# Performance work log

Measured on AMD Instinct MI355X. Metric: run time of the kernel, lower is better.

Reference implementation:

```python
import jax, jax.numpy as jnp
import numpy as np

N = 8192
IN_F = 512
OUT_F = 64
ALPHA = 0.2  # LeakyReLU negative slope
NEG_INF = -9e15


def setup_inputs() -> dict:
    key = jax.random.key(0)
    k1, k2, k3, k4 = jax.random.split(key, 4)
    # xavier_uniform-style scale (gain=1.414)
    w_bound = 1.414 * np.sqrt(6.0 / (IN_F + OUT_F))
    a_bound = 1.414 * np.sqrt(6.0 / (2 * OUT_F + 1))
    return {
        "input": jax.random.normal(k1, (N, IN_F), dtype=jnp.float32),
        "adj": jax.random.randint(k2, (N, N), 0, 2, dtype=jnp.int32),
        "W": jax.random.uniform(k3, (IN_F, OUT_F), jnp.float32, -w_bound, w_bound),
        "a": jax.random.uniform(k4, (2 * OUT_F, 1), jnp.float32, -a_bound, a_bound),
        "sig_sample_size": 512,
    }


def reference(input, adj, W, a, sig_sample_size):
    h = input @ W  # [N, F]
    # Split 'a' so e_ij = leakyrelu(a1.h_i + a2.h_j) without the N*N*2F repeat/cat
    a1, a2 = a[:OUT_F, 0], a[OUT_F:, 0]  # [F], [F]
    e = jax.nn.leaky_relu((h @ a1)[:, None] + (h @ a2)[None, :], negative_slope=ALPHA)  # [N, N]
    attention = jnp.where(adj > 0, e, NEG_INF)
    attention = jax.nn.softmax(attention, axis=1)
    sig_scores = jnp.sum(attention, axis=0)  # [N]
    _, indices = jax.lax.top_k(sig_scores, sig_sample_size)
    return indices
```

## Files before the change

### kernel.cpp

```cpp
#include <hip/hip_runtime.h>
#include <stdint.h>

#define NROW 8192
#define IN_F 512
#define OUT_F 64
#define ALPHA 0.2f

__device__ float  g_wa1[IN_F];
__device__ float  g_wa2[IN_F];
__device__ float  g_f1[NROW];
__device__ float  g_f2[NROW];
__device__ float  g_E2f[NROW];
__device__ float  g_F2f[NROW];
__device__ double g_E2d[NROW];
__device__ double g_F2d[NROW];
__device__ double g_accp[NROW];
__device__ double g_accn[NROW];
__device__ double g_G1[NROW];
__device__ double g_H1[NROW];
__device__ double g_colsum[NROW];
__device__ unsigned long long g_mask[(size_t)NROW * 128];

__global__ void prep_wa(const float* __restrict__ W, const float* __restrict__ a) {
    int k = threadIdx.x;
    if (k < IN_F) {
        double s1 = 0.0, s2 = 0.0;
        for (int t = 0; t < OUT_F; ++t) {
            double w = (double)W[k * OUT_F + t];
            s1 += w * (double)a[t];
            s2 += w * (double)a[OUT_F + t];
        }
        g_wa1[k] = (float)s1;
        g_wa2[k] = (float)s2;
        #pragma unroll
        for (int i = 0; i < 16; ++i) g_colsum[k * 16 + i] = 0.0;
    }
}

__global__ void __launch_bounds__(256) compute_f(const float* __restrict__ in) {
    int wave = threadIdx.x >> 6, lane = threadIdx.x & 63;
    int row = blockIdx.x * 4 + wave;
    const float4* in4  = (const float4*)(in + (size_t)row * IN_F);
    const float4* wa14 = (const float4*)g_wa1;
    const float4* wa24 = (const float4*)g_wa2;
    double s1 = 0.0, s2 = 0.0;
    #pragma unroll
    for (int half = 0; half < 2; ++half) {
        int idx = half * 64 + lane;
        float4 x = in4[idx];
        float4 u = wa14[idx];
        float4 v = wa24[idx];
        s1 += (double)x.x*u.x + (double)x.y*u.y + (double)x.z*u.z + (double)x.w*u.w;
        s2 += (double)x.x*v.x + (double)x.y*v.y + (double)x.z*v.z + (double)x.w*v.w;
    }
    #pragma unroll
    for (int off = 32; off > 0; off >>= 1) {
        s1 += __shfl_down(s1, off, 64);
        s2 += __shfl_down(s2, off, 64);
    }
    if (lane == 0) {
        float f1 = (float)s1, f2 = (float)s2;
        g_f1[row] = f1; g_f2[row] = f2;
        double e2 = exp((double)f2), g2 = exp(0.2 * (double)f2);
        g_E2d[row] = e2;        g_F2d[row] = g2;
        g_E2f[row] = (float)e2; g_F2f[row] = (float)g2;
    }
}

__global__ void __launch_bounds__(256) row_z_mask(const int* __restrict__ adj) {
    __shared__ float E2s[NROW];
    __shared__ float F2s[NROW];
    __shared__ double zp[16], zn[16];
    int tid = threadIdx.x;
    int wave = tid >> 6, lane = tid & 63;
    for (int k = tid; k < NROW / 4; k += 256) {
        ((float4*)E2s)[k] = ((const float4*)g_E2f)[k];
        ((float4*)F2s)[k] = ((const float4*)g_F2f)[k];
    }
    __syncthreads();
    int row0 = blockIdx.x * 4;
    for (int r = 0; r < 4; ++r) {
        int row = row0 + r;
        float f1r = g_f1[row];
        float Ft = expf(-0.2f * f1r);
        const int4* arow = (const int4*)(adj + (size_t)row * NROW) + wave * 512;
        unsigned long long myword = 0;
        double accp = 0.0, accn = 0.0;
        #pragma unroll
        for (int it = 0; it < 8; ++it) {
            int4 av = arow[it * 64 + lane];
            int colbase = wave * 2048 + it * 256 + lane * 4;
            float4 E2v = *(const float4*)&E2s[colbase];
            float4 F2v = *(const float4*)&F2s[colbase];
            bool p0 = av.x > 0, p1 = av.y > 0, p2 = av.z > 0, p3 = av.w > 0;
            unsigned long long b0 = __ballot(p0), b1 = __ballot(p1);
            unsigned long long b2 = __ballot(p2), b3 = __ballot(p3);
            int bl = it * 4;
            if (lane == bl)     myword = b0;
            if (lane == bl + 1) myword = b1;
            if (lane == bl + 2) myword = b2;
            if (lane == bl + 3) myword = b3;
            bool q0 = F2v.x > Ft, q1 = F2v.y > Ft, q2 = F2v.z > Ft, q3 = F2v.w > Ft;
            accp += (p0 && q0) ? (double)E2v.x : 0.0;
            accn += (p0 && !q0) ? (double)F2v.x : 0.0;
            accp += (p1 && q1) ? (double)E2v.y : 0.0;
            accn += (p1 && !q1) ? (double)F2v.y : 0.0;
            accp += (p2 && q2) ? (double)E2v.z : 0.0;
            accn += (p2 && !q2) ? (double)F2v.z : 0.0;
            accp += (p3 && q3) ? (double)E2v.w : 0.0;
            accn += (p3 && !q3) ? (double)F2v.w : 0.0;
        }
        if (lane < 32) g_mask[(size_t)row * 128 + wave * 32 + lane] = myword;
        #pragma unroll
        for (int off = 32; off > 0; off >>= 1) {
            accp += __shfl_down(accp, off, 64);
            accn += __shfl_down(accn, off, 64);
        }
        if (lane == 0) { zp[r * 4 + wave] = accp; zn[r * 4 + wave] = accn; }
    }
    __syncthreads();
    if (tid < 4) {
        g_accp[row0 + tid] = zp[tid*4+0] + zp[tid*4+1] + zp[tid*4+2] + zp[tid*4+3];
        g_accn[row0 + tid] = zn[tid*4+0] + zn[tid*4+1] + zn[tid*4+2] + zn[tid*4+3];
    }
}

__global__ void __launch_bounds__(256) prep_gh() {
    int i = blockIdx.x * 256 + threadIdx.x;
    double f1d = (double)g_f1[i];
    double e1 = exp(f1d), h1 = exp(0.2 * f1d);
    double Z = e1 * g_accp[i] + h1 * g_accn[i];
    double zinv = 1.0 / Z;
    g_G1[i] = e1 * zinv;
    g_H1[i] = h1 * zinv;
}

__global__ void __launch_bounds__(256) colsum_kernel() {
    __shared__ float  f1s[256];
    __shared__ double G1s[256], H1s[256];
    __shared__ unsigned long long msk[1024];
    int tid = threadIdx.x;
    int cb = blockIdx.x & 31;
    int rb = blockIdx.x >> 5;
    int j = cb * 256 + tid;
    float f2j = g_f2[j];
    int i0 = rb * 256;
    f1s[tid] = g_f1[i0 + tid];
    G1s[tid] = g_G1[i0 + tid];
    H1s[tid] = g_H1[i0 + tid];
    for (int t = tid; t < 1024; t += 256)
        msk[t] = g_mask[(size_t)(i0 + (t >> 2)) * 128 + cb * 4 + (t & 3)];
    __syncthreads();
    int c = tid & 3, bit = (tid >> 2) & 63;
    double accp = 0.0, accn = 0.0;
    for (int i = 0; i < 256; ++i) {
        unsigned long long wv = msk[i * 4 + c];
        bool b = (wv >> bit) & 1ULL;
        float e = f1s[i] + f2j;
        bool pos = e > 0.0f;
        accp += (b && pos)  ? G1s[i] : 0.0;
        accn += (b && !pos) ? H1s[i] : 0.0;
    }
    double res = g_E2d[j] * accp + g_F2d[j] * accn;
    atomicAdd(&g_colsum[j], res);
}

__global__ void __launch_bounds__(1024) topk_kernel(int* __restrict__ out, int K) {
    __shared__ unsigned int sbits[NROW];
    __shared__ unsigned int hist[256];
    __shared__ unsigned long long cand[1024];
    __shared__ unsigned long long s_prefix;
    __shared__ unsigned int s_want, s_cnt;
    int tid = threadIdx.x;
    for (int k = tid; k < NROW; k += 1024) {
        float s = (float)g_colsum[k];
        unsigned int u = __float_as_uint(s);
        u = (u & 0x80000000u) ? ~u : (u | 0x80000000u);
        sbits[k] = u;
    }
    if (tid == 0) { s_prefix = 0ULL; s_want = (unsigned)K; s_cnt = 0; }
    __syncthreads();
    for (int lvl = 0; lvl < 6; ++lvl) {
        int shift = 40 - lvl * 8;
        if (tid < 256) hist[tid] = 0;
        __syncthreads();
        unsigned long long pmask = (lvl == 0) ? 0ULL : (~0ULL << (shift + 8));
        unsigned long long prefix = s_prefix;
        for (int k = tid; k < NROW; k += 1024) {
            unsigned long long kk =
                ((unsigned long long)sbits[k] << 13) | (unsigned long long)(8191 - k);
            if ((kk & pmask) == prefix)
                atomicAdd(&hist[(unsigned)(kk >> shift) & 255u], 1u);
        }
        __syncthreads();
        if (tid == 0) {
            unsigned cum = 0; int b = 255;
            for (; b >= 0; --b) { cum += hist[b]; if (cum >= s_want) break; }
            if (b < 0) b = 0;
            s_want -= (cum - hist[b]);
            s_prefix |= ((unsigned long long)b << shift);
        }
        __syncthreads();
    }
    unsigned long long thr = s_prefix;
    for (int k = tid; k < NROW; k += 1024) {
        unsigned long long kk =
            ((unsigned long long)sbits[k] << 13) | (unsigned long long)(8191 - k);
        if (kk >= thr) {
            unsigned pos = atomicAdd(&s_cnt, 1u);
            if (pos < 1024u) cand[pos] = kk;
        }
    }
    __syncthreads();
    unsigned cnt = s_cnt;
    if ((unsigned)tid >= cnt) cand[tid] = 0ULL;
    __syncthreads();
    for (int k2 = 2; k2 <= 1024; k2 <<= 1) {
        for (int jj = k2 >> 1; jj > 0; jj >>= 1) {
            int ixj = tid ^ jj;
            if (ixj > tid) {
                unsigned long long a = cand[tid], b = cand[ixj];
                bool up = ((tid & k2) == 0);
                if (up ? (a < b) : (a > b)) { cand[tid] = b; cand[ixj] = a; }
            }
            __syncthreads();
        }
    }
    if (tid < K) out[tid] = 8191 - (int)(cand[tid] & 0x1FFFULL);
}

extern "C" void kernel_launch(void* const* d_in, const int* in_sizes, int n_in,
                              void* d_out, int out_size, void* d_ws, size_t ws_size,
                              hipStream_t stream) {
    const float* input = (const float*)d_in[0];
    const int*   adj   = (const int*)d_in[1];
    const float* W     = (const float*)d_in[2];
    const float* a     = (const float*)d_in[3];
    int* out = (int*)d_out;
    int K = out_size;

    prep_wa<<<1, 512, 0, stream>>>(W, a);
    compute_f<<<NROW / 4, 256, 0, stream>>>(input);
    row_z_mask<<<NROW / 4, 256, 0, stream>>>(adj);
    prep_gh<<<NROW / 256, 256, 0, stream>>>();
    colsum_kernel<<<1024, 256, 0, stream>>>();
    topk_kernel<<<1, 1024, 0, stream>>>(out, K);
}
```

Baseline: 513.4 us.

## Fuse W·a prep into f-computation and fold softmax normalizer into row kernel

Merges prep_wa into compute_f: every block recomputes the 512-element W·a vectors into shared memory and zeroes its own slice of the colsum buffer. The per-row exp/normalization that prep_gh did now runs at the tail of row_z_mask, which drops the accp/accn global arrays. This removes two kernel launches and their global round trips. The cost is 2048 blocks each redoing the small W·a matvec (512x64 reads of W from cache) instead of doing it once.

```diff
diff --git a/kernel.cpp b/kernel.cpp
--- a/kernel.cpp
+++ b/kernel.cpp
@@ -6,43 +6,45 @@
 #define OUT_F 64
 #define ALPHA 0.2f
 
-__device__ float  g_wa1[IN_F];
-__device__ float  g_wa2[IN_F];
 __device__ float  g_f1[NROW];
 __device__ float  g_f2[NROW];
 __device__ float  g_E2f[NROW];
 __device__ float  g_F2f[NROW];
 __device__ double g_E2d[NROW];
 __device__ double g_F2d[NROW];
-__device__ double g_accp[NROW];
-__device__ double g_accn[NROW];
 __device__ double g_G1[NROW];
 __device__ double g_H1[NROW];
 __device__ double g_colsum[NROW];
 __device__ unsigned long long g_mask[(size_t)NROW * 128];
 
-__global__ void prep_wa(const float* __restrict__ W, const float* __restrict__ a) {
-    int k = threadIdx.x;
-    if (k < IN_F) {
+__global__ void __launch_bounds__(256) setup_kernel(const float* __restrict__ in,
+                                                    const float* __restrict__ W,
+                                                    const float* __restrict__ a) {
+    __shared__ float swa1[IN_F];
+    __shared__ float swa2[IN_F];
+    int tid = threadIdx.x;
+    #pragma unroll
+    for (int kk = 0; kk < 2; ++kk) {
+        int k = tid + kk * 256;
         double s1 = 0.0, s2 = 0.0;
-        for (int t = 0; t < OUT_F; ++t) {
-            double w = (double)W[k * OUT_F + t];
-            s1 += w * (double)a[t];
-            s2 += w * (double)a[OUT_F + t];
-        }
-        g_wa1[k] = (float)s1;
-        g_wa2[k] = (float)s2;
-        #pragma unroll
-        for (int i = 0; i < 16; ++i) g_colsum[k * 16 + i] = 0.0;
-    }
-}
-
-__global__ void __launch_bounds__(256) compute_f(const float* __restrict__ in) {
-    int wave = threadIdx.x >> 6, lane = threadIdx.x & 63;
+        for (int t = 0; t < OUT_F; t += 4) {
+            float4 w = *(const float4*)&W[k * OUT_F + t];
+            s1 += (double)w.x * (double)a[t]     + (double)w.y * (double)a[t + 1]
+                + (double)w.z * (double)a[t + 2] + (double)w.w * (double)a[t + 3];
+            s2 += (double)w.x * (double)a[OUT_F + t]     + (double)w.y * (double)a[OUT_F + t + 1]
+                + (double)w.z * (double)a[OUT_F + t + 2] + (double)w.w * (double)a[OUT_F + t + 3];
+        }
+        swa1[k] = (float)s1;
+        swa2[k] = (float)s2;
+    }
+    if (tid < 4) g_colsum[blockIdx.x * 4 + tid] = 0.0;
+    __syncthreads();
+
+    int wave = tid >> 6, lane = tid & 63;
     int row = blockIdx.x * 4 + wave;
     const float4* in4  = (const float4*)(in + (size_t)row * IN_F);
-    const float4* wa14 = (const float4*)g_wa1;
-    const float4* wa24 = (const float4*)g_wa2;
+    const float4* wa14 = (const float4*)swa1;
+    const float4* wa24 = (const float4*)swa2;
     double s1 = 0.0, s2 = 0.0;
     #pragma unroll
     for (int half = 0; half < 2; ++half) {
@@ -120,19 +122,15 @@
     }
     __syncthreads();
     if (tid < 4) {
-        g_accp[row0 + tid] = zp[tid*4+0] + zp[tid*4+1] + zp[tid*4+2] + zp[tid*4+3];
-        g_accn[row0 + tid] = zn[tid*4+0] + zn[tid*4+1] + zn[tid*4+2] + zn[tid*4+3];
-    }
-}
-
-__global__ void __launch_bounds__(256) prep_gh() {
-    int i = blockIdx.x * 256 + threadIdx.x;
-    double f1d = (double)g_f1[i];
-    double e1 = exp(f1d), h1 = exp(0.2 * f1d);
-    double Z = e1 * g_accp[i] + h1 * g_accn[i];
-    double zinv = 1.0 / Z;
-    g_G1[i] = e1 * zinv;
-    g_H1[i] = h1 * zinv;
+        int row = row0 + tid;
+        double accp = zp[tid*4+0] + zp[tid*4+1] + zp[tid*4+2] + zp[tid*4+3];
+        double accn = zn[tid*4+0] + zn[tid*4+1] + zn[tid*4+2] + zn[tid*4+3];
+        double f1d = (double)g_f1[row];
+        double e1 = exp(f1d), h1 = exp(0.2 * f1d);
+        double zinv = 1.0 / (e1 * accp + h1 * accn);
+        g_G1[row] = e1 * zinv;
+        g_H1[row] = h1 * zinv;
+    }
 }
 
 __global__ void __launch_bounds__(256) colsum_kernel() {
@@ -239,10 +237,8 @@
     int* out = (int*)d_out;
     int K = out_size;
 
-    prep_wa<<<1, 512, 0, stream>>>(W, a);
-    compute_f<<<NROW / 4, 256, 0, stream>>>(input);
+    setup_kernel<<<NROW / 4, 256, 0, stream>>>(input, W, a);
     row_z_mask<<<NROW / 4, 256, 0, stream>>>(adj);
-    prep_gh<<<NROW / 256, 256, 0, stream>>>();
     colsum_kernel<<<1024, 256, 0, stream>>>();
     topk_kernel<<<1, 1024, 0, stream>>>(out, K);
 }
```

Measured after the change: 530.6 us. 1.03x slower.
